# Kernel optimization log

Hardware: AMD Instinct MI355X
Metric: run time of the kernel (lower is better)

The kernel has to match this reference:

```python
import jax, jax.numpy as jnp
import numpy as np

B, NL, NP, E = 64, 128, 128, 4096


def setup_inputs() -> dict:
    key = jax.random.key(0)
    k1, k2, k3, k4, k5 = jax.random.split(key, 5)
    P = jax.random.uniform(k1, (B, NL, NP), dtype=jnp.float32)
    # normalize rows so P looks like soft assignment probabilities
    P = P / P.sum(-1, keepdims=True)
    d_error = jax.random.uniform(k2, (NP, NP), dtype=jnp.float32)
    edge_weights = jax.random.uniform(k3, (B, E), dtype=jnp.float32)
    d_hw = jax.random.randint(k4, (NP, NP), 0, 6, dtype=jnp.int32)
    edge_pairs = jax.random.randint(k5, (B, E, 2), 0, NL, dtype=jnp.int64)
    return {"P": P, "d_error": d_error, "edge_weights": edge_weights,
            "d_hw": d_hw, "edge_pairs": edge_pairs}


def reference(P, d_error, edge_weights, d_hw, edge_pairs):
    # A_fidelity = adjacency (d_hw == 1) weighted by clamped fidelity
    A_fid = (d_hw == 1).astype(P.dtype) * jnp.maximum(1.0 - d_error, 0.0)  # [Np,Np]
    i = edge_pairs[..., 0]  # [B,E]
    j = edge_pairs[..., 1]  # [B,E]
    Pi = jnp.take_along_axis(P, i[..., None], axis=1)  # [B,E,Np] gather of P[b,i,:]
    Pj = jnpp = jnp.take_along_axis(P, j[..., None], axis=1)  # [B,E,Np]
    # per-edge score: P[b,i,:] @ A_fid @ P[b,j,:]
    scores = jnp.einsum('bep,pq,beq->be', Pi, A_fid, Pj)
    w_sum = jnp.maximum(edge_weights.sum(-1), 1e-8)  # [B]
    sample_adj = (edge_weights * scores).sum(-1) / w_sum  # [B]
    # all samples have edges -> valid_samples == B
    loss = -sample_adj.mean()
    return loss
```

## Files before the change

### kernel.cpp

```cpp
#include <hip/hip_runtime.h>
#include <hip/hip_bf16.h>

#define B_   64
#define NL_  128
#define NP_  128
#define E_   4096


__global__ __launch_bounds__(256) void k_prep(
    const float* __restrict__ d_error,
    const int*   __restrict__ d_hw,
    const float* __restrict__ ew,
    const int*   __restrict__ pairs_raw,
    float* __restrict__ A,
    float* __restrict__ Wt,
    float* __restrict__ den)
{
    const int blk  = blockIdx.x;
    const int b    = blk >> 1;
    const int half = blk & 1;
    const int t    = threadIdx.x;

    if (t < 128) {
        int idx = blk * 128 + t;
        A[idx] = (d_hw[idx] == 1) ? fmaxf(1.0f - d_error[idx], 0.0f) : 0.0f;
    }

    int hwv = pairs_raw[2 * (t & 63) + 1];
    unsigned long long nz = __ballot(hwv != 0);
    const int is64 = (nz == 0ULL);

    const float* wrow = ew + (size_t)b * E_ + half * 2048;

    {
        const float4* ew4 = (const float4*)wrow;
        float4 v0 = ew4[t];
        float4 v1 = ew4[t + 256];
        float s = v0.x + v0.y + v0.z + v0.w + v1.x + v1.y + v1.z + v1.w;
        #pragma unroll
        for (int off = 32; off >= 1; off >>= 1) s += __shfl_xor(s, off, 64);
        __shared__ float rs[4];
        if ((t & 63) == 0) rs[t >> 6] = s;
        __syncthreads();
        if (t == 0) atomicAdd(&den[b], rs[0] + rs[1] + rs[2] + rs[3]);
    }

    float* Wb = Wt + (size_t)b * (NL_ * NL_);
    if (is64) {
        const int4* pp = (const int4*)pairs_raw + (size_t)b * E_ + half * 2048;
        #pragma unroll 4
        for (int k = 0; k < 8; ++k) {
            int e = k * 256 + t;
            int4 pr = pp[e];
            atomicAdd(&Wb[pr.z * NL_ + pr.x], wrow[e]);
        }
    } else {
        const int2* pp = (const int2*)pairs_raw + (size_t)b * E_ + half * 2048;
        #pragma unroll 4
        for (int k = 0; k < 8; ++k) {
            int e = k * 256 + t;
            int2 pr = pp[e];
            atomicAdd(&Wb[pr.y * NL_ + pr.x], wrow[e]);
        }
    }
}

__global__ __launch_bounds__(256) void k_main(
    const float* __restrict__ P,
    const float* __restrict__ A,
    const float* __restrict__ Wt,
    float* __restrict__ num_part)
{
    const int b     = blockIdx.x >> 3;
    const int chunk = blockIdx.x & 7;
    const int r0    = chunk * 16;
    const int t  = threadIdx.x;
    const int tr = t >> 5;
    const int tc = t & 31;

    const float* Pb  = P + (size_t)b * NL_ * NP_;
    const float* Pr0 = Pb + (size_t)(r0 + 2*tr) * NP_;
    const float* Pr1 = Pr0 + NP_;

    const float4* A4 = (const float4*)A;
    float4 q0 = {0,0,0,0}, q1 = {0,0,0,0};
    #pragma unroll 8
    for (int p = 0; p < NP_; ++p) {
        float4 av = A4[p * 32 + tc];
        float pv0 = Pr0[p];
        float pv1 = Pr1[p];
        q0.x = fmaf(pv0, av.x, q0.x); q0.y = fmaf(pv0, av.y, q0.y);
        q0.z = fmaf(pv0, av.z, q0.z); q0.w = fmaf(pv0, av.w, q0.w);
        q1.x = fmaf(pv1, av.x, q1.x); q1.y = fmaf(pv1, av.y, q1.y);
        q1.z = fmaf(pv1, av.z, q1.z); q1.w = fmaf(pv1, av.w, q1.w);
    }

    const float2* W2 = (const float2*)(Wt + (size_t)b * (NL_ * NL_));
    const float4* P4 = (const float4*)Pb;
    const int wof = (r0 >> 1) + tr;
    float4 ra0 = {0,0,0,0}, ra1 = {0,0,0,0};
    #pragma unroll 8
    for (int lp = 0; lp < NL_; ++lp) {
        float2 w01 = W2[lp * 64 + wof];
        float4 pv  = P4[lp * 32 + tc];
        ra0.x = fmaf(w01.x, pv.x, ra0.x); ra0.y = fmaf(w01.x, pv.y, ra0.y);
        ra0.z = fmaf(w01.x, pv.z, ra0.z); ra0.w = fmaf(w01.x, pv.w, ra0.w);
        ra1.x = fmaf(w01.y, pv.x, ra1.x); ra1.y = fmaf(w01.y, pv.y, ra1.y);
        ra1.z = fmaf(w01.y, pv.z, ra1.z); ra1.w = fmaf(w01.y, pv.w, ra1.w);
    }

    float nacc = q0.x*ra0.x + q0.y*ra0.y + q0.z*ra0.z + q0.w*ra0.w
               + q1.x*ra1.x + q1.y*ra1.y + q1.z*ra1.z + q1.w*ra1.w;
    #pragma unroll
    for (int off = 32; off >= 1; off >>= 1) nacc += __shfl_xor(nacc, off, 64);
    __shared__ float red[4];
    if ((t & 63) == 0) red[t >> 6] = nacc;
    __syncthreads();
    if (t == 0) num_part[blockIdx.x] = red[0] + red[1] + red[2] + red[3];
}

__global__ __launch_bounds__(64) void k_final(
    const float* __restrict__ num_part,
    const float* __restrict__ den,
    float* __restrict__ out)
{
    int b = threadIdx.x;
    float n = 0.0f;
    #pragma unroll
    for (int c = 0; c < 8; ++c) n += num_part[b * 8 + c];
    float v = n / fmaxf(den[b], 1e-8f);
    #pragma unroll
    for (int off = 32; off >= 1; off >>= 1) v += __shfl_xor(v, off, 64);
    if (b == 0) out[0] = -v / (float)B_;
}

extern "C" void kernel_launch(void* const* d_in, const int* in_sizes, int n_in,
                              void* d_out, int out_size, void* d_ws, size_t ws_size,
                              hipStream_t stream) {
    const float* P       = (const float*)d_in[0];
    const float* d_error = (const float*)d_in[1];
    const float* ew      = (const float*)d_in[2];
    const int*   d_hw    = (const int*)d_in[3];
    const int*   pairs   = (const int*)d_in[4];
    float* out = (float*)d_out;

    char*  ws  = (char*)d_ws;
    float* Wt  = (float*)ws;
    float* den = (float*)(ws + 4194304);
    float* num = (float*)(ws + 4194560);
    float* A   = (float*)(ws + 4196608);

    hipMemsetAsync(ws, 0, 4194560, stream);

    k_prep <<<128, 256, 0, stream>>>(d_error, d_hw, ew, pairs, A, Wt, den);
    k_main <<<512, 256, 0, stream>>>(P, A, Wt, num);
    k_final<<<1,   64,  0, stream>>>(num, den, out);
}
```

Measured before the change: 107.6 us.

## Build per-batch weight matrix in LDS, drop the workspace memset

Each of the 64 blocks (1024 threads) now accumulates the 128x128 edge-weight scatter matrix for one batch in shared memory with LDS atomics, then writes it to global memory with coalesced float4 stores. The batch weight sum is written directly rather than accumulated atomically. Together these remove the 4 MB hipMemsetAsync and the global atomics. The cost is fewer, larger blocks (64 instead of 128) that each use 64 KB of LDS, which lowers parallelism in the prep stage.

```diff
diff --git a/kernel.cpp b/kernel.cpp
--- a/kernel.cpp
+++ b/kernel.cpp
@@ -7,7 +7,7 @@
 #define E_   4096
 
 
-__global__ __launch_bounds__(256) void k_prep(
+__global__ __launch_bounds__(1024) void k_wbuild(
     const float* __restrict__ d_error,
     const int*   __restrict__ d_hw,
     const float* __restrict__ ew,
@@ -16,53 +16,63 @@
     float* __restrict__ Wt,
     float* __restrict__ den)
 {
-    const int blk  = blockIdx.x;
-    const int b    = blk >> 1;
-    const int half = blk & 1;
-    const int t    = threadIdx.x;
+    __shared__ float WT[NL_ * NL_];
+    __shared__ float rs[16];
+    const int b = blockIdx.x;
+    const int t = threadIdx.x;
 
-    if (t < 128) {
-        int idx = blk * 128 + t;
+    float4* WT4 = (float4*)WT;
+    #pragma unroll
+    for (int k = 0; k < 4; ++k) WT4[k * 1024 + t] = float4{0, 0, 0, 0};
+
+    if (t < 256) {
+        int idx = b * 256 + t;
         A[idx] = (d_hw[idx] == 1) ? fmaxf(1.0f - d_error[idx], 0.0f) : 0.0f;
+    }
+
+    const float* wrow = ew + (size_t)b * E_;
+    {
+        float4 v = ((const float4*)wrow)[t];
+        float s = v.x + v.y + v.z + v.w;
+        #pragma unroll
+        for (int off = 32; off >= 1; off >>= 1) s += __shfl_xor(s, off, 64);
+        if ((t & 63) == 0) rs[t >> 6] = s;
     }
 
     int hwv = pairs_raw[2 * (t & 63) + 1];
     unsigned long long nz = __ballot(hwv != 0);
     const int is64 = (nz == 0ULL);
+    __syncthreads();
 
-    const float* wrow = ew + (size_t)b * E_ + half * 2048;
-
-    {
-        const float4* ew4 = (const float4*)wrow;
-        float4 v0 = ew4[t];
-        float4 v1 = ew4[t + 256];
-        float s = v0.x + v0.y + v0.z + v0.w + v1.x + v1.y + v1.z + v1.w;
+    if (t == 0) {
+        float s = 0.0f;
         #pragma unroll
-        for (int off = 32; off >= 1; off >>= 1) s += __shfl_xor(s, off, 64);
-        __shared__ float rs[4];
-        if ((t & 63) == 0) rs[t >> 6] = s;
-        __syncthreads();
-        if (t == 0) atomicAdd(&den[b], rs[0] + rs[1] + rs[2] + rs[3]);
+        for (int k = 0; k < 16; ++k) s += rs[k];
+        den[b] = s;
     }
 
-    float* Wb = Wt + (size_t)b * (NL_ * NL_);
     if (is64) {
-        const int4* pp = (const int4*)pairs_raw + (size_t)b * E_ + half * 2048;
-        #pragma unroll 4
-        for (int k = 0; k < 8; ++k) {
-            int e = k * 256 + t;
+        const int4* pp = (const int4*)pairs_raw + (size_t)b * E_;
+        #pragma unroll
+        for (int k = 0; k < 4; ++k) {
+            int e = k * 1024 + t;
             int4 pr = pp[e];
-            atomicAdd(&Wb[pr.z * NL_ + pr.x], wrow[e]);
+            atomicAdd(&WT[pr.z * NL_ + pr.x], wrow[e]);
         }
     } else {
-        const int2* pp = (const int2*)pairs_raw + (size_t)b * E_ + half * 2048;
-        #pragma unroll 4
-        for (int k = 0; k < 8; ++k) {
-            int e = k * 256 + t;
+        const int2* pp = (const int2*)pairs_raw + (size_t)b * E_;
+        #pragma unroll
+        for (int k = 0; k < 4; ++k) {
+            int e = k * 1024 + t;
             int2 pr = pp[e];
-            atomicAdd(&Wb[pr.y * NL_ + pr.x], wrow[e]);
+            atomicAdd(&WT[pr.y * NL_ + pr.x], wrow[e]);
         }
     }
+    __syncthreads();
+
+    float4* Wg4 = (float4*)(Wt + (size_t)b * (NL_ * NL_));
+    #pragma unroll
+    for (int k = 0; k < 4; ++k) Wg4[k * 1024 + t] = WT4[k * 1024 + t];
 }
 
 __global__ __launch_bounds__(256) void k_main(
@@ -150,9 +160,7 @@
     float* num = (float*)(ws + 4194560);
     float* A   = (float*)(ws + 4196608);
 
-    hipMemsetAsync(ws, 0, 4194560, stream);
-
-    k_prep <<<128, 256, 0, stream>>>(d_error, d_hw, ew, pairs, A, Wt, den);
-    k_main <<<512, 256, 0, stream>>>(P, A, Wt, num);
-    k_final<<<1,   64,  0, stream>>>(num, den, out);
+    k_wbuild<<<64,  1024, 0, stream>>>(d_error, d_hw, ew, pairs, A, Wt, den);
+    k_main  <<<512, 256,  0, stream>>>(P, A, Wt, num);
+    k_final <<<1,   64,   0, stream>>>(num, den, out);
 }
```

New measurement: 99.63 us. 1.08x faster.
